# Kernel tuning notes

Measured on AMD Instinct MI355X. Metric: run time of the kernel, lower is better.

The kernel has to match this reference:

```python
import jax, jax.numpy as jnp
import numpy as np
from math import sqrt

EPS = 1e-5


def _head_branch(x, W, b, a, g, be):
    # x: (B,C,T,F); W: (H,O,C); b: (H,O); a: (H,) PReLU; g,be: (H,1,O,1,F)
    y = jnp.einsum('bctf,hoc->hbotf', x, W) + b[:, None, :, None, None]
    y = jnp.where(y > 0, y, a[:, None, None, None, None] * y)  # PReLU
    mean = y.mean(axis=(2, 4), keepdims=True)                  # ChannelNorm over (C,F)
    var = y.var(axis=(2, 4), keepdims=True)
    return (y - mean) / jnp.sqrt(var + EPS) * g + be           # (H,B,O,T,F)


def _proj(x, W, b, a, g, be):
    # x: (B,C,T,F); W: (C,C); b: (C,); a: scalar; g,be: (1,C,1,F)
    y = jnp.einsum('bctf,oc->botf', x, W) + b[None, :, None, None]
    y = jnp.where(y > 0, y, a * y)
    mean = y.mean(axis=(1, 3), keepdims=True)
    var = y.var(axis=(1, 3), keepdims=True)
    return (y - mean) / jnp.sqrt(var + EPS) * g + be


def setup_inputs() -> dict:
    key = jax.random.key(0)
    ks = jax.random.split(key, 8)
    B, C, T, F, H, HID = 4, 64, 1024, 128, 4, 4
    CH = C // H
    x = jax.random.normal(ks[0], (B, C, T, F), dtype=jnp.float32)
    Wq = jax.random.normal(ks[1], (H, HID, C), dtype=jnp.float32) * 0.05
    Wk = jax.random.normal(ks[2], (H, HID, C), dtype=jnp.float32) * 0.05
    Wv = jax.random.normal(ks[3], (H, CH, C), dtype=jnp.float32) * 0.05
    Wp = jax.random.normal(ks[4], (C, C), dtype=jnp.float32) * 0.05
    return {
        'x': x,
        'Wq': Wq, 'bq': jnp.zeros((H, HID)), 'aq': jnp.full((H,), 0.25),
        'gq': jnp.ones((H, 1, HID, 1, F)), 'betaq': jnp.zeros((H, 1, HID, 1, F)),
        'Wk': Wk, 'bk': jnp.zeros((H, HID)), 'ak': jnp.full((H,), 0.25),
        'gk': jnp.ones((H, 1, HID, 1, F)), 'betak': jnp.zeros((H, 1, HID, 1, F)),
        'Wv': Wv, 'bv': jnp.zeros((H, CH)), 'av': jnp.full((H,), 0.25),
        'gv': jnp.ones((H, 1, CH, 1, F)), 'betav': jnp.zeros((H, 1, CH, 1, F)),
        'Wp': Wp, 'bp': jnp.zeros((C,)), 'ap': jnp.float32(0.25),
        'gp': jnp.ones((1, C, 1, F)), 'betap': jnp.zeros((1, C, 1, F)),
    }


def reference(x, Wq, bq, aq, gq, betaq, Wk, bk, ak, gk, betak,
              Wv, bv, av, gv, betav, Wp, bp, ap, gp, betap):
    B, C, T, F = x.shape
    H = Wq.shape[0]
    CH = C // H
    q = _head_branch(x, Wq, bq, aq, gq, betaq)   # (H,B,HID,T,F)
    k = _head_branch(x, Wk, bk, ak, gk, betak)   # (H,B,HID,T,F)
    v = _head_branch(x, Wv, bv, av, gv, betav)   # (H,B,CH,T,F)
    # cat(dim=0) head-major, transpose(1,2), flatten -> (H*B, T, O*F)
    qf = q.transpose(0, 1, 3, 2, 4).reshape(H * B, T, -1)
    kf = k.transpose(0, 1, 3, 2, 4).reshape(H * B, T, -1)
    vf = v.transpose(0, 1, 3, 2, 4).reshape(H * B, T, -1)
    scale = 1.0 / sqrt(qf.shape[-1])
    attn = jax.nn.softmax(jnp.einsum('nqd,nkd->nqk', qf, kf) * scale, axis=-1)
    out = jnp.einsum('nqk,nkd->nqd', attn, vf)   # (H*B, T, CH*F)
    # invert torch's view/transpose chain back to (B,C,T,F)
    out = out.reshape(H, B, T, CH, F).transpose(1, 0, 3, 2, 4).reshape(B, C, T, F)
    out = _proj(out, Wp, bp, ap, gp, betap)
    return out + x
```

## Files before the change

### kernel.cpp

```cpp
#include <hip/hip_runtime.h>
#include <hip/hip_bf16.h>

typedef __attribute__((ext_vector_type(4))) float f32x4;
typedef __attribute__((ext_vector_type(8))) short short8;

__device__ __forceinline__ float bf2f(unsigned short u){
  union { unsigned u32; float f; } v; v.u32 = ((unsigned)u) << 16; return v.f;
}
__device__ __forceinline__ unsigned short f2bf(float f){
  union { float f; unsigned u; } v; v.f = f;
  unsigned x = v.u;
  unsigned r = x + 0x7fffu + ((x >> 16) & 1u);
  return (unsigned short)(r >> 16);
}
__device__ __forceinline__ short8 pack8(f32x4 a, f32x4 b){
  short8 r;
  r[0]=(short)f2bf(a[0]); r[1]=(short)f2bf(a[1]);
  r[2]=(short)f2bf(a[2]); r[3]=(short)f2bf(a[3]);
  r[4]=(short)f2bf(b[0]); r[5]=(short)f2bf(b[1]);
  r[6]=(short)f2bf(b[2]); r[7]=(short)f2bf(b[3]);
  return r;
}

__global__ __launch_bounds__(256) void prep_kernel(
    const float* bq, const float* aq, const float* bk, const float* ak,
    const float* bv, const float* av, const float* Wp,
    float* ball, float* aall, float* Wps)
{
  int idx = blockIdx.x * 256 + threadIdx.x;
  if (idx < 96) {
    int j = idx;
    float b, a;
    if (j < 16)      { b = bq[j];      a = aq[j >> 2]; }
    else if (j < 32) { b = bk[j - 16]; a = ak[(j - 16) >> 2]; }
    else             { b = bv[j - 32]; a = av[(j - 32) >> 4]; }
    ball[j] = b; aall[j] = a;
  } else if (idx < 96 + 4096) {
    int r = idx - 96; int o = r >> 6, c = r & 63;
    Wps[c * 64 + o] = Wp[o * 64 + c];
  }
}

__global__ __launch_bounds__(256, 2) void qkv_mfma(
    const float* __restrict__ x,
    const float* __restrict__ Wq, const float* __restrict__ Wk,
    const float* __restrict__ Wv,
    const float* __restrict__ ball, const float* __restrict__ aall,
    const float* __restrict__ gq, const float* __restrict__ gk,
    const float* __restrict__ gv,
    const float* __restrict__ beq, const float* __restrict__ bek,
    const float* __restrict__ bev,
    unsigned short* __restrict__ qf, unsigned short* __restrict__ kf,
    unsigned short* __restrict__ vf)
{
  __shared__ unsigned short upool[96 * 264];
  __shared__ float partS[4][96], partQ[4][96];
  __shared__ float gm[2][12], gi[2][12];
  __shared__ float bias_l[96], a_l[96];

  int tid = threadIdx.x;
  int t0 = blockIdx.x * 2, b = blockIdx.y;
  int lane = tid & 63, wave = tid >> 6;
  int l15 = lane & 15, quad = lane >> 4;

  if (tid < 96) { bias_l[tid] = ball[tid]; a_l[tid] = aall[tid]; }

  const float* wsrc[6] = {
    Wq + l15 * 64, Wk + l15 * 64,
    Wv + l15 * 64, Wv + (16 + l15) * 64,
    Wv + (32 + l15) * 64, Wv + (48 + l15) * 64
  };
  short8 afr[6][2];
  #pragma unroll
  for (int mt = 0; mt < 6; mt++)
    #pragma unroll
    for (int ks = 0; ks < 2; ks++) {
      const float* p = wsrc[mt] + ks * 32 + quad * 8;
      afr[mt][ks] = pack8(*(const f32x4*)p, *(const f32x4*)(p + 4));
    }

  unsigned short* xl = upool;
  #pragma unroll
  for (int it = 0; it < 4; it++) {
    int item = it * 256 + tid;
    int cb = item >> 7;
    int np = item & 127;
    int n = np * 2;
    int tl = n >> 7, f = n & 127;
    const float* gp = x + ((long)(b * 64 + cb * 8) * 1024 + t0 + tl) * 128 + f;
    short8 lo, hi;
    #pragma unroll
    for (int w = 0; w < 8; w++) {
      float2 v = *(const float2*)(gp + (long)w * 131072);
      lo[w] = (short)f2bf(v.x);
      hi[w] = (short)f2bf(v.y);
    }
    int perm = cb ^ (np & 7);
    *(short8*)&xl[n * 64 + perm * 8]       = lo;
    *(short8*)&xl[(n + 1) * 64 + perm * 8] = hi;
  }
  __syncthreads();

  f32x4 acc[6][4];
  #pragma unroll
  for (int mt = 0; mt < 6; mt++)
    #pragma unroll
    for (int nt = 0; nt < 4; nt++)
      acc[mt][nt] = {0.f, 0.f, 0.f, 0.f};

  int nb = wave * 64;
  #pragma unroll
  for (int ks = 0; ks < 2; ks++)
    #pragma unroll
    for (int nt = 0; nt < 4; nt++) {
      int n = nb + nt * 16 + l15;
      int perm = (ks * 4 + quad) ^ ((n >> 1) & 7);
      short8 bfrag = *(const short8*)&xl[n * 64 + perm * 8];
      #pragma unroll
      for (int mt = 0; mt < 6; mt++)
        acc[mt][nt] = __builtin_amdgcn_mfma_f32_16x16x32_bf16(
            afr[mt][ks], bfrag, acc[mt][nt], 0, 0, 0);
    }

  #pragma unroll
  for (int mt = 0; mt < 6; mt++)
    #pragma unroll
    for (int r = 0; r < 4; r++) {
      int j = mt * 16 + quad * 4 + r;
      float bb = bias_l[j], aa = a_l[j];
      #pragma unroll
      for (int nt = 0; nt < 4; nt++) {
        float v = acc[mt][nt][r] + bb;
        acc[mt][nt][r] = v > 0.f ? v : aa * v;
      }
      float s  = acc[mt][0][r] + acc[mt][1][r] + acc[mt][2][r] + acc[mt][3][r];
      float q2 = acc[mt][0][r]*acc[mt][0][r] + acc[mt][1][r]*acc[mt][1][r]
               + acc[mt][2][r]*acc[mt][2][r] + acc[mt][3][r]*acc[mt][3][r];
      #pragma unroll
      for (int m = 1; m <= 8; m <<= 1) {
        s  += __shfl_xor(s,  m, 64);
        q2 += __shfl_xor(q2, m, 64);
      }
      if (l15 == 0) { partS[wave][j] = s; partQ[wave][j] = q2; }
    }
  __syncthreads();

  unsigned short* yl = upool;
  #pragma unroll
  for (int mt = 0; mt < 6; mt++)
    #pragma unroll
    for (int nt = 0; nt < 4; nt++) {
      int n = nb + nt * 16 + l15;
      #pragma unroll
      for (int r = 0; r < 4; r++) {
        int j = mt * 16 + quad * 4 + r;
        yl[j * 264 + n] = f2bf(acc[mt][nt][r]);
      }
    }
  if (tid < 24) {
    int g = tid % 12, tl2 = tid / 12;
    int r0 = (g < 4) ? g * 4 : (g < 8) ? 16 + (g - 4) * 4 : 32 + (g - 8) * 16;
    int nr = (g < 8) ? 4 : 16;
    float S = 0.f, Q = 0.f;
    for (int w = tl2 * 2; w < tl2 * 2 + 2; w++)
      for (int r = 0; r < nr; r++) { S += partS[w][r0 + r]; Q += partQ[w][r0 + r]; }
    float cnt = (float)(nr * 128);
    float mean = S / cnt;
    float var = fmaxf(Q / cnt - mean * mean, 0.f);
    gm[tl2][g] = mean;
    gi[tl2][g] = rsqrtf(var + 1e-5f);
  }
  __syncthreads();

  int ch = tid & 31, jrow = tid >> 5;
  #pragma unroll
  for (int itj = 0; itj < 12; itj++) {
    int j = itj * 8 + jrow;
    int n0 = ch * 8;
    int tl3 = n0 >> 7, f = n0 & 127;
    short8 y8 = *(const short8*)&yl[j * 264 + n0];
    int g = (j < 16) ? (j >> 2) : (j < 32) ? 4 + ((j - 16) >> 2) : 8 + ((j - 32) >> 4);
    float mean = gm[tl3][g], inv = gi[tl3][g];
    const float *gsrc, *bsrc;
    int jo;
    unsigned short* dst;
    if (j < 16) {
      jo = j; gsrc = gq; bsrc = beq;
      int h = j >> 2, o = j & 3;
      dst = qf + (((long)(h * 4 + b) * 1024 + t0 + tl3) * 512 + o * 128 + f);
    } else if (j < 32) {
      jo = j - 16; gsrc = gk; bsrc = bek;
      int h = jo >> 2, o = jo & 3;
      dst = kf + (((long)(h * 4 + b) * 1024 + t0 + tl3) * 512 + o * 128 + f);
    } else {
      jo = j - 32; gsrc = gv; bsrc = bev;
      int h = jo >> 4, o = jo & 15;
      dst = vf + (((long)(h * 4 + b) * 1024 + t0 + tl3) * 2048 + o * 128 + f);
    }
    f32x4 g0 = *(const f32x4*)(gsrc + jo * 128 + f);
    f32x4 g1 = *(const f32x4*)(gsrc + jo * 128 + f + 4);
    f32x4 b0 = *(const f32x4*)(bsrc + jo * 128 + f);
    f32x4 b1 = *(const f32x4*)(bsrc + jo * 128 + f + 4);
    short8 o8;
    #pragma unroll
    for (int i = 0; i < 4; i++) {
      o8[i]     = (short)f2bf((bf2f((unsigned short)y8[i])     - mean) * inv * g0[i] + b0[i]);
      o8[i + 4] = (short)f2bf((bf2f((unsigned short)y8[i + 4]) - mean) * inv * g1[i] + b1[i]);
    }
    *(short8*)dst = o8;
  }
}

__global__ __launch_bounds__(256) void transpose_v(
    const unsigned short* __restrict__ vf, unsigned short* __restrict__ vfT)
{
  __shared__ unsigned short tile[64][65];
  int n = blockIdx.z;
  int d0 = blockIdx.x * 64, t0 = blockIdx.y * 64;
  int tid = threadIdx.x;
  int cr = tid >> 4, cc = (tid & 15) * 4;

  const unsigned short* src = vf + ((long)n * 1024 + t0) * 2048 + d0;
  #pragma unroll
  for (int i = 0; i < 4; i++) {
    int r = cr + i * 16;
    ushort4 u = *(const ushort4*)(src + (long)r * 2048 + cc);
    tile[r][cc + 0] = u.x; tile[r][cc + 1] = u.y;
    tile[r][cc + 2] = u.z; tile[r][cc + 3] = u.w;
  }
  __syncthreads();
  unsigned short* dst = vfT + ((long)n * 2048 + d0) * 1024 + t0;
  #pragma unroll
  for (int i = 0; i < 4; i++) {
    int r = cr + i * 16;
    ushort4 u;
    u.x = tile[cc + 0][r]; u.y = tile[cc + 1][r];
    u.z = tile[cc + 2][r]; u.w = tile[cc + 3][r];
    *(ushort4*)(dst + (long)r * 1024 + cc) = u;
  }
}

__global__ __launch_bounds__(256) void gemm_bt(
    const unsigned short* __restrict__ A, const unsigned short* __restrict__ B,
    unsigned short* __restrict__ Cb, float* __restrict__ Cf,
    int M, int N, int K, long sA, long sB, long sC, float scale, int mode)
{
  __shared__ unsigned short As[128 * 40];
  __shared__ unsigned short Bs[128 * 40];
  int tid = threadIdx.x;
  int z = blockIdx.z;
  int m0 = blockIdx.y * 128, n0 = blockIdx.x * 128;
  const unsigned short* Ab = A + (long)z * sA + (long)m0 * K;
  const unsigned short* Bb = B + (long)z * sB + (long)n0 * K;
  int lane = tid & 63, wave = tid >> 6;
  int wm = (wave >> 1) * 64, wn = (wave & 1) * 64;
  int l15 = lane & 15, quad = lane >> 4;

  f32x4 acc[4][4];
  #pragma unroll
  for (int i = 0; i < 4; i++)
    #pragma unroll
    for (int j = 0; j < 4; j++) acc[i][j] = {0.f, 0.f, 0.f, 0.f};

  for (int k0 = 0; k0 < K; k0 += 32) {
    #pragma unroll
    for (int i = 0; i < 2; i++) {
      int id = tid + i * 256;
      int row = id >> 2, c8 = (id & 3) * 8;
      *(short8*)&As[row * 40 + c8] = *(const short8*)(Ab + (long)row * K + k0 + c8);
      *(short8*)&Bs[row * 40 + c8] = *(const short8*)(Bb + (long)row * K + k0 + c8);
    }
    __syncthreads();
    short8 af[4], bfr[4];
    #pragma unroll
    for (int i = 0; i < 4; i++)
      af[i] = *(const short8*)&As[(wm + i * 16 + l15) * 40 + quad * 8];
    #pragma unroll
    for (int j = 0; j < 4; j++)
      bfr[j] = *(const short8*)&Bs[(wn + j * 16 + l15) * 40 + quad * 8];
    #pragma unroll
    for (int i = 0; i < 4; i++)
      #pragma unroll
      for (int j = 0; j < 4; j++)
        acc[i][j] = __builtin_amdgcn_mfma_f32_16x16x32_bf16(af[i], bfr[j], acc[i][j], 0, 0, 0);
    __syncthreads();
  }

  if (mode == 0) {
    #pragma unroll
    for (int i = 0; i < 4; i++)
      #pragma unroll
      for (int j = 0; j < 4; j++) {
        int row = m0 + wm + i * 16 + quad * 4;
        int col = n0 + wn + j * 16 + l15;
        unsigned short* cp = Cb + (long)z * sC + (long)row * N + col;
        #pragma unroll
        for (int r = 0; r < 4; r++)
          cp[(long)r * N] = f2bf(acc[i][j][r] * scale);
      }
  } else {
    int bb = z & 3, h = z >> 2;
    #pragma unroll
    for (int i = 0; i < 4; i++)
      #pragma unroll
      for (int j = 0; j < 4; j++) {
        int row = m0 + wm + i * 16 + quad * 4;
        int col = n0 + wn + j * 16 + l15;
        int c = col >> 7, f = col & 127;
        float* cp = Cf + (((long)(bb * 64 + h * 16 + c) * 1024 + row) * 128 + f);
        #pragma unroll
        for (int r = 0; r < 4; r++)
          cp[(long)r * 128] = acc[i][j][r];
      }
  }
}

__global__ __launch_bounds__(256) void softmax_kernel(unsigned short* __restrict__ P)
{
  __shared__ float red[4];
  __shared__ float bmax, bsum;
  int row = blockIdx.x, z = blockIdx.y, tid = threadIdx.x;
  unsigned short* p = P + ((long)z * 1024 + row) * 1024;
  ushort4 u = *(ushort4*)(p + tid * 4);
  float v0 = bf2f(u.x), v1 = bf2f(u.y), v2 = bf2f(u.z), v3 = bf2f(u.w);

  float m = fmaxf(fmaxf(v0, v1), fmaxf(v2, v3));
  #pragma unroll
  for (int s = 1; s <= 32; s <<= 1) m = fmaxf(m, __shfl_xor(m, s, 64));
  if ((tid & 63) == 0) red[tid >> 6] = m;
  __syncthreads();
  if (tid == 0) bmax = fmaxf(fmaxf(red[0], red[1]), fmaxf(red[2], red[3]));
  __syncthreads();
  m = bmax;

  float e0 = __expf(v0 - m), e1 = __expf(v1 - m), e2 = __expf(v2 - m), e3 = __expf(v3 - m);
  float s = e0 + e1 + e2 + e3;
  #pragma unroll
  for (int k = 1; k <= 32; k <<= 1) s += __shfl_xor(s, k, 64);
  if ((tid & 63) == 0) red[tid >> 6] = s;
  __syncthreads();
  if (tid == 0) bsum = red[0] + red[1] + red[2] + red[3];
  __syncthreads();
  float inv = 1.0f / bsum;

  u.x = f2bf(e0 * inv); u.y = f2bf(e1 * inv);
  u.z = f2bf(e2 * inv); u.w = f2bf(e3 * inv);
  *(ushort4*)(p + tid * 4) = u;
}

__global__ __launch_bounds__(256) void proj_kernel(
    float* __restrict__ io, const float* __restrict__ Wps,
    const float* __restrict__ bp, const float* __restrict__ ap,
    const float* __restrict__ gp, const float* __restrict__ bep,
    const float* __restrict__ x)
{
  __shared__ float xl[64 * 128];
  __shared__ float wl[64 * 64];
  __shared__ float redS[4], redQ[4];
  __shared__ float smean, sinv;

  int tid = threadIdx.x;
  int t = blockIdx.x, b = blockIdx.y;

  float* src = io + ((long)(b * 64) * 1024 + t) * 128;
  #pragma unroll
  for (int i = 0; i < 8; i++) {
    int id = tid + i * 256;
    int c = id >> 5, f4 = (id & 31) * 4;
    *(f32x4*)&xl[c * 128 + f4] = *(const f32x4*)(src + (long)c * 131072 + f4);
  }
  #pragma unroll
  for (int i = 0; i < 4; i++) {
    int id = tid + i * 256;
    ((f32x4*)wl)[id] = ((const f32x4*)Wps)[id];
  }
  __syncthreads();

  int fblk = tid & 31, rblk = tid >> 5;
  int f0 = fblk * 4, r0 = rblk * 8;

  float acc[8][4];
  #pragma unroll
  for (int rr = 0; rr < 8; rr++)
    #pragma unroll
    for (int ff = 0; ff < 4; ff++) acc[rr][ff] = 0.f;

  for (int c = 0; c < 64; c++) {
    f32x4 xv = *(const f32x4*)&xl[c * 128 + f0];
    f32x4 w0 = *(const f32x4*)&wl[c * 64 + r0];
    f32x4 w1 = *(const f32x4*)&wl[c * 64 + r0 + 4];
    #pragma unroll
    for (int rr = 0; rr < 4; rr++) {
      #pragma unroll
      for (int ff = 0; ff < 4; ff++) {
        acc[rr][ff]     += w0[rr] * xv[ff];
        acc[rr + 4][ff] += w1[rr] * xv[ff];
      }
    }
  }

  float aval = ap[0];
  #pragma unroll
  for (int rr = 0; rr < 8; rr++) {
    float bb = bp[r0 + rr];
    #pragma unroll
    for (int ff = 0; ff < 4; ff++) {
      float v = acc[rr][ff] + bb;
      acc[rr][ff] = v > 0.f ? v : aval * v;
    }
  }

  float s = 0.f, sq = 0.f;
  #pragma unroll
  for (int rr = 0; rr < 8; rr++)
    #pragma unroll
    for (int ff = 0; ff < 4; ff++) { s += acc[rr][ff]; sq += acc[rr][ff] * acc[rr][ff]; }
  #pragma unroll
  for (int m = 1; m <= 32; m <<= 1) { s += __shfl_xor(s, m, 64); sq += __shfl_xor(sq, m, 64); }
  if ((tid & 63) == 0) { redS[tid >> 6] = s; redQ[tid >> 6] = sq; }
  __syncthreads();
  if (tid == 0) {
    float S = redS[0] + redS[1] + redS[2] + redS[3];
    float Q = redQ[0] + redQ[1] + redQ[2] + redQ[3];
    float mean = S / 8192.0f;
    float var = fmaxf(Q / 8192.0f - mean * mean, 0.f);
    smean = mean; sinv = rsqrtf(var + 1e-5f);
  }
  __syncthreads();
  float mean = smean, inv = sinv;

  const float* xb = x + ((long)(b * 64) * 1024 + t) * 128;
  #pragma unroll
  for (int rr = 0; rr < 8; rr++) {
    int c = r0 + rr;
    f32x4 g4 = *(const f32x4*)(gp + c * 128 + f0);
    f32x4 b4 = *(const f32x4*)(bep + c * 128 + f0);
    f32x4 x4 = *(const f32x4*)(xb + (long)c * 131072 + f0);
    f32x4 o;
    o[0] = (acc[rr][0] - mean) * inv * g4[0] + b4[0] + x4[0];
    o[1] = (acc[rr][1] - mean) * inv * g4[1] + b4[1] + x4[1];
    o[2] = (acc[rr][2] - mean) * inv * g4[2] + b4[2] + x4[2];
    o[3] = (acc[rr][3] - mean) * inv * g4[3] + b4[3] + x4[3];
    *(f32x4*)(io + ((long)(b * 64 + c) * 1024 + t) * 128 + f0) = o;
  }
}

extern "C" void kernel_launch(void* const* d_in, const int* in_sizes, int n_in,
                              void* d_out, int out_size, void* d_ws, size_t ws_size,
                              hipStream_t stream)
{
  const float* x   = (const float*)d_in[0];
  const float* Wq  = (const float*)d_in[1];
  const float* bq  = (const float*)d_in[2];
  const float* aq  = (const float*)d_in[3];
  const float* gq  = (const float*)d_in[4];
  const float* beq = (const float*)d_in[5];
  const float* Wk  = (const float*)d_in[6];
  const float* bk  = (const float*)d_in[7];
  const float* ak  = (const float*)d_in[8];
  const float* gk  = (const float*)d_in[9];
  const float* bek = (const float*)d_in[10];
  const float* Wv  = (const float*)d_in[11];
  const float* bv  = (const float*)d_in[12];
  const float* av  = (const float*)d_in[13];
  const float* gv  = (const float*)d_in[14];
  const float* bev = (const float*)d_in[15];
  const float* Wp  = (const float*)d_in[16];
  const float* bp  = (const float*)d_in[17];
  const float* ap  = (const float*)d_in[18];
  const float* gp  = (const float*)d_in[19];
  const float* bep = (const float*)d_in[20];
  float* out = (float*)d_out;

  char* ws = (char*)d_ws;
  size_t off = 0;
  auto alloc = [&](size_t n) { size_t o = off; off += (n + 255) & ~(size_t)255; return o; };

  float* ball = (float*)(ws + alloc(96 * 4));
  float* aall = (float*)(ws + alloc(96 * 4));
  float* Wps  = (float*)(ws + alloc(4096 * 4));
  unsigned short* qf  = (unsigned short*)(ws + alloc((size_t)16 * 1024 * 512 * 2));
  unsigned short* kf  = (unsigned short*)(ws + alloc((size_t)16 * 1024 * 512 * 2));
  unsigned short* vf  = (unsigned short*)(ws + alloc((size_t)16 * 1024 * 2048 * 2));
  unsigned short* vfT = (unsigned short*)(ws + alloc((size_t)16 * 1024 * 2048 * 2));
  unsigned short* P   = vf;

  prep_kernel<<<17, 256, 0, stream>>>(bq, aq, bk, ak, bv, av, Wp,
                                      ball, aall, Wps);

  qkv_mfma<<<dim3(512, 4), 256, 0, stream>>>(
      x, Wq, Wk, Wv, ball, aall, gq, gk, gv, beq, bek, bev, qf, kf, vf);

  transpose_v<<<dim3(32, 16, 16), 256, 0, stream>>>(vf, vfT);

  gemm_bt<<<dim3(8, 8, 16), 256, 0, stream>>>(
      qf, kf, P, (float*)nullptr, 1024, 1024, 512,
      (long)1024 * 512, (long)1024 * 512, (long)1024 * 1024,
      0.04419417382f , 0);

  softmax_kernel<<<dim3(1024, 16), 256, 0, stream>>>(P);

  gemm_bt<<<dim3(16, 8, 16), 256, 0, stream>>>(
      P, vfT, (unsigned short*)nullptr, out, 1024, 2048, 1024,
      (long)1024 * 1024, (long)2048 * 1024, 0, 1.0f, 1);

  proj_kernel<<<dim3(1024, 4), 256, 0, stream>>>(out, Wps, bp, ap, gp, bep, x);
}
```

Measured before the change: 588.3 us.

## Load GEMM tiles directly into LDS with XOR swizzle and XCD-aware tile remap

```diff
diff --git a/kernel.cpp b/kernel.cpp
--- a/kernel.cpp
+++ b/kernel.cpp
@@ -20,6 +20,12 @@
   r[4]=(short)f2bf(b[0]); r[5]=(short)f2bf(b[1]);
   r[6]=(short)f2bf(b[2]); r[7]=(short)f2bf(b[3]);
   return r;
+}
+
+__device__ __forceinline__ void gload_lds16(const unsigned short* g, unsigned short* l) {
+  __builtin_amdgcn_global_load_lds(
+      (const __attribute__((address_space(1))) unsigned int*)g,
+      (__attribute__((address_space(3))) unsigned int*)l, 16, 0, 0);
 }
 
 __global__ __launch_bounds__(256) void prep_kernel(
@@ -245,11 +251,19 @@
     unsigned short* __restrict__ Cb, float* __restrict__ Cf,
     int M, int N, int K, long sA, long sB, long sC, float scale, int mode)
 {
-  __shared__ unsigned short As[128 * 40];
-  __shared__ unsigned short Bs[128 * 40];
+  __shared__ unsigned short As[128 * 32];
+  __shared__ unsigned short Bs[128 * 32];
   int tid = threadIdx.x;
-  int z = blockIdx.z;
-  int m0 = blockIdx.y * 128, n0 = blockIdx.x * 128;
+
+  int gx = gridDim.x, gy = gridDim.y;
+  int bid = blockIdx.x + gx * (blockIdx.y + gy * blockIdx.z);
+  int nwg = gx * gy * (int)gridDim.z;
+  int cpx = nwg >> 3;
+  int tile = (bid & 7) * cpx + (bid >> 3);
+  int tx = tile % gx, trem = tile / gx;
+  int ty = trem % gy, z = trem / gy;
+
+  int m0 = ty * 128, n0 = tx * 128;
   const unsigned short* Ab = A + (long)z * sA + (long)m0 * K;
   const unsigned short* Bb = B + (long)z * sB + (long)n0 * K;
   int lane = tid & 63, wave = tid >> 6;
@@ -262,22 +276,29 @@
     #pragma unroll
     for (int j = 0; j < 4; j++) acc[i][j] = {0.f, 0.f, 0.f, 0.f};
 
+  int srow = lane >> 2;
+  int sck  = (lane & 3) ^ (srow & 3);
+
   for (int k0 = 0; k0 < K; k0 += 32) {
     #pragma unroll
-    for (int i = 0; i < 2; i++) {
-      int id = tid + i * 256;
-      int row = id >> 2, c8 = (id & 3) * 8;
-      *(short8*)&As[row * 40 + c8] = *(const short8*)(Ab + (long)row * K + k0 + c8);
-      *(short8*)&Bs[row * 40 + c8] = *(const short8*)(Bb + (long)row * K + k0 + c8);
+    for (int it = 0; it < 2; it++) {
+      int R = it * 64 + wave * 16;
+      int row = R + srow;
+      gload_lds16(Ab + (long)row * K + k0 + sck * 8, &As[R * 32]);
+      gload_lds16(Bb + (long)row * K + k0 + sck * 8, &Bs[R * 32]);
     }
     __syncthreads();
     short8 af[4], bfr[4];
     #pragma unroll
-    for (int i = 0; i < 4; i++)
-      af[i] = *(const short8*)&As[(wm + i * 16 + l15) * 40 + quad * 8];
-    #pragma unroll
-    for (int j = 0; j < 4; j++)
-      bfr[j] = *(const short8*)&Bs[(wn + j * 16 + l15) * 40 + quad * 8];
+    for (int i = 0; i < 4; i++) {
+      int row = wm + i * 16 + l15;
+      af[i] = *(const short8*)&As[row * 32 + (quad ^ (row & 3)) * 8];
+    }
+    #pragma unroll
+    for (int j = 0; j < 4; j++) {
+      int row = wn + j * 16 + l15;
+      bfr[j] = *(const short8*)&Bs[row * 32 + (quad ^ (row & 3)) * 8];
+    }
     #pragma unroll
     for (int i = 0; i < 4; i++)
       #pragma unroll
```

New measurement: 593.2 us. About the same (+0.8%).
